# Kernel optimization log

Hardware: AMD Instinct MI355X
Metric: run time of the kernel (lower is better)

Reference implementation:

```python
import jax, jax.numpy as jnp
import numpy as np
import math

B, C, H, W = 4, 256, 64, 64
E = 96  # embed_dim
SOFTMAX_SCALE = 10.0
RESIDUAL_SCALE_INIT = 0.1


def conv1x1(w, x):
    # w: [out_c, in_c], x: [b, in_c, h, w] -> [b, out_c, h, w]
    return jnp.einsum('oc,bchw->bohw', w, x)


def setup_inputs() -> dict:
    key = jax.random.key(0)
    ks = jax.random.split(key, 12)
    s = 0.02
    return {
        'x': jax.random.normal(ks[0], (B, C, H, W), jnp.float32),
        'mask': jax.random.uniform(ks[1], (B, 1, H, W), jnp.float32),
        'ln_gamma': jnp.ones((C,), jnp.float32),
        'ln_beta': jnp.zeros((C,), jnp.float32),
        'wq': jax.random.normal(ks[2], (E, C), jnp.float32) * s,
        'wk': jax.random.normal(ks[3], (E, C), jnp.float32) * s,
        'wv': jax.random.normal(ks[4], (C, C), jnp.float32) * s,
        'w_out': jax.random.normal(ks[5], (C, C), jnp.float32) * s,
        'w_qm': jax.random.normal(ks[6], (E, 1), jnp.float32) * s,
        'wd1': jax.random.normal(ks[7], (C, 2 * C), jnp.float32) * s,
        'wd2': jax.random.normal(ks[8], (C, C), jnp.float32) * s,
        'wg': jax.random.normal(ks[9], (C, C + 1), jnp.float32) * s,
        'residual_scale': jnp.asarray(RESIDUAL_SCALE_INIT, jnp.float32),
    }


def reference(x, mask, ln_gamma, ln_beta, wq, wk, wv, w_out, w_qm, wd1, wd2, wg,
              residual_scale):
    b, c, h, w = x.shape
    n = h * w

    # ChannelLayerNorm: LayerNorm over channel dim
    mu = jnp.mean(x, axis=1, keepdims=True)
    var = jnp.mean((x - mu) ** 2, axis=1, keepdims=True)
    x_norm = (x - mu) / jnp.sqrt(var + 1e-5)
    x_norm = x_norm * ln_gamma[None, :, None, None] + ln_beta[None, :, None, None]

    # Q/K/V projections (1x1 convs), flatten to [b, n, d]
    q = conv1x1(wq, x_norm) + conv1x1(w_qm, mask)
    q = q.reshape(b, E, n).transpose(0, 2, 1)        # [b, n, E]
    k = conv1x1(wk, x_norm).reshape(b, E, n).transpose(0, 2, 1)  # [b, n, E]
    v = conv1x1(wv, x).reshape(b, c, n).transpose(0, 2, 1)       # [b, n, C]

    # cosine normalization (F.normalize with eps=1e-12)
    q = q / jnp.clip(jnp.linalg.norm(q, axis=-1, keepdims=True), 1e-12)
    k = k / jnp.clip(jnp.linalg.norm(k, axis=-1, keepdims=True), 1e-12)

    scale = SOFTMAX_SCALE / math.sqrt(E)
    attn = jnp.einsum('bqe,bke->bqk', q, k) * scale  # [b, n, n]

    # keys with mask >= 0.5 are invalid -> bias -10000
    invalid_keys = (mask.reshape(b, 1, n) >= 0.5)    # [b, 1, n]
    attn = jnp.where(invalid_keys, jnp.float32(-10000.0), attn)
    attn = jax.nn.softmax(attn, axis=-1)

    attended = jnp.einsum('bqk,bkc->bqc', attn, v)   # [b, n, C]
    attended = attended.transpose(0, 2, 1).reshape(b, c, h, w)
    attended = conv1x1(w_out, attended)

    # delta correction branch
    corr_in = jnp.concatenate([attended - x, x_norm * mask], axis=1)  # [b, 2C, h, w]
    hidden = jax.nn.gelu(conv1x1(wd1, corr_in), approximate=False)
    corrective = conv1x1(wd2, hidden)

    # MaskConditionedGate (assumed): sigmoid(1x1 conv over [corrective, mask])
    gate_in = jnp.concatenate([corrective, mask], axis=1)  # [b, C+1, h, w]
    gate = jax.nn.sigmoid(conv1x1(wg, gate_in)) * mask

    delta = jnp.tanh(residual_scale) * gate * corrective
    return x + delta
```

## Files before the change

kernel.cpp:

```cpp
#include <hip/hip_runtime.h>
#include <hip/hip_bf16.h>
#include <math.h>

#define BB 4
#define CC 256
#define NN 4096
#define EE 96
#define NTOT (BB*NN)

typedef __attribute__((ext_vector_type(8))) short bf16x8;
typedef __attribute__((ext_vector_type(4))) float f32x4;

__device__ __forceinline__ short f2bf(float x) {
    __hip_bfloat16 h = __float2bfloat16(x);
    return *reinterpret_cast<short*>(&h);
}
__device__ __forceinline__ float bf2f(short s) {
    unsigned int u = ((unsigned int)(unsigned short)s) << 16;
    float f;
    __builtin_memcpy(&f, &u, 4);
    return f;
}
__device__ __forceinline__ float gelu_exact(float v) {
    return 0.5f * v * (1.0f + erff(v * 0.70710678118654752f));
}
__device__ __forceinline__ void gld16(void* lds, const void* g) {
    __builtin_amdgcn_global_load_lds(
        (const __attribute__((address_space(1))) unsigned int*)g,
        (__attribute__((address_space(3))) unsigned int*)lds, 16, 0, 0);
}

#define OFF_WQ  0
#define OFF_WK  24576
#define OFF_WV  49152
#define OFF_WO  114688
#define OFF_WD1 180224
#define OFF_WD2 311296
#define OFF_WG  376832
#define OFF_WGL 442368
#define W16_TOTAL 442624

__global__ void wconv_kernel(const float* __restrict__ wq, const float* __restrict__ wk,
                             const float* __restrict__ wv, const float* __restrict__ wo,
                             const float* __restrict__ wd1, const float* __restrict__ wd2,
                             const float* __restrict__ wg, short* __restrict__ W16) {
    int i = blockIdx.x * 256 + threadIdx.x;
    if (i >= W16_TOTAL) return;
    float v;
    if      (i < OFF_WK)  v = wq[i];
    else if (i < OFF_WV)  v = wk[i - OFF_WK];
    else if (i < OFF_WO)  v = wv[i - OFF_WV];
    else if (i < OFF_WD1) v = wo[i - OFF_WO];
    else if (i < OFF_WD2) v = wd1[i - OFF_WD1];
    else if (i < OFF_WG)  v = wd2[i - OFF_WD2];
    else if (i < OFF_WGL) { int l = i - OFF_WG; v = wg[(l >> 8) * 257 + (l & 255)]; }
    else                  v = wg[(i - OFF_WGL) * 257 + 256];
    W16[i] = f2bf(v);
}

__global__ __launch_bounds__(256) void ln_kernel(
    const float* __restrict__ x, const float* __restrict__ gamma,
    const float* __restrict__ beta,
    short* __restrict__ Xt16, short* __restrict__ Xn16) {
    __shared__ float tile[256 * 33];
    __shared__ float psum[8][32], psq[8][32];
    __shared__ float mu_s[32], rs_s[32];
    __shared__ float gs[256], bs[256];
    const int b  = blockIdx.x >> 7;
    const int p0 = (blockIdx.x & 127) * 32;
    const int tid = threadIdx.x;
    const float* xb = x + (size_t)b * CC * NN;

    gs[tid] = gamma[tid];
    bs[tid] = beta[tid];
    #pragma unroll
    for (int i = 0; i < 8; ++i) {
        int idx = tid + i * 256;
        int c = idx >> 3, p4 = (idx & 7) * 4;
        float4 v = *(const float4*)&xb[(size_t)c * NN + p0 + p4];
        tile[c * 33 + p4]     = v.x;
        tile[c * 33 + p4 + 1] = v.y;
        tile[c * 33 + p4 + 2] = v.z;
        tile[c * 33 + p4 + 3] = v.w;
    }
    __syncthreads();
    {
        int col = tid & 31, part = tid >> 5;
        float s = 0.f, sq = 0.f;
        for (int r = part * 32; r < part * 32 + 32; ++r) {
            float v = tile[r * 33 + col];
            s += v; sq += v * v;
        }
        psum[part][col] = s; psq[part][col] = sq;
    }
    __syncthreads();
    if (tid < 32) {
        float S = 0.f, SQ = 0.f;
        #pragma unroll
        for (int j = 0; j < 8; ++j) { S += psum[j][tid]; SQ += psq[j][tid]; }
        float mu = S / 256.0f;
        float var = SQ / 256.0f - mu * mu;
        mu_s[tid] = mu;
        rs_s[tid] = rsqrtf(var + 1e-5f);
    }
    __syncthreads();
    size_t rowbase = ((size_t)b * NN + p0) * CC;
    #pragma unroll
    for (int i = 0; i < 4; ++i) {
        int idx = tid + i * 256;
        int p = idx >> 5, c8 = (idx & 31) * 8;
        float mu = mu_s[p], rcp = rs_s[p];
        bf16x8 xt, xn;
        #pragma unroll
        for (int j = 0; j < 8; ++j) {
            float v = tile[(c8 + j) * 33 + p];
            float n = (v - mu) * rcp * gs[c8 + j] + bs[c8 + j];
            xt[j] = f2bf(v); xn[j] = f2bf(n);
        }
        size_t o = rowbase + (size_t)p * CC + c8;
        *(bf16x8*)&Xt16[o] = xt;
        *(bf16x8*)&Xn16[o] = xn;
    }
}

__global__ __launch_bounds__(256) void qkproj_kernel(
    const short* __restrict__ Xn16, const short* __restrict__ W16,
    const float* __restrict__ mask, const float* __restrict__ w_qm,
    short* __restrict__ Q16, short* __restrict__ K16)
{
    const int tid = threadIdx.x;
    const int w = tid >> 6, lane = tid & 63, ln = lane & 15, quad = lane >> 4;
    const int m0 = blockIdx.x * 32 + (w & 1) * 16;
    const bool isQ = (w < 2);
    const int woff = isQ ? OFF_WQ : OFF_WK;

    f32x4 acc[6];
    #pragma unroll
    for (int i = 0; i < 6; ++i) acc[i] = (f32x4){0.f, 0.f, 0.f, 0.f};

    #pragma unroll
    for (int kt = 0; kt < 8; ++kt) {
        bf16x8 af = *(const bf16x8*)&Xn16[(size_t)(m0 + ln) * 256 + kt * 32 + quad * 8];
        #pragma unroll
        for (int nt = 0; nt < 6; ++nt) {
            bf16x8 bf = *(const bf16x8*)&W16[woff + (size_t)(nt * 16 + ln) * 256 + kt * 32 + quad * 8];
            acc[nt] = __builtin_amdgcn_mfma_f32_16x16x32_bf16(af, bf, acc[nt], 0, 0, 0);
        }
    }

    short* outp = isQ ? Q16 : K16;
    #pragma unroll
    for (int r = 0; r < 4; ++r) {
        int row = m0 + quad * 4 + r;
        float mrow = isQ ? mask[row] : 0.f;
        float vals[6];
        float ss = 0.f;
        #pragma unroll
        for (int nt = 0; nt < 6; ++nt) {
            float v = acc[nt][r];
            if (isQ) v += mrow * w_qm[nt * 16 + ln];
            vals[nt] = v;
            ss += v * v;
        }
        ss += __shfl_xor(ss, 1, 64); ss += __shfl_xor(ss, 2, 64);
        ss += __shfl_xor(ss, 4, 64); ss += __shfl_xor(ss, 8, 64);
        float sc = 1.0f / fmaxf(sqrtf(ss), 1e-12f);
        #pragma unroll
        for (int nt = 0; nt < 6; ++nt)
            outp[(size_t)row * EE + nt * 16 + ln] = f2bf(vals[nt] * sc);
    }
}

__global__ __launch_bounds__(256) void vproj_kernel(
    const short* __restrict__ Xt16, const short* __restrict__ W16,
    short* __restrict__ V16t)
{
    __shared__ short Vt[256 * 40];
    const int tid = threadIdx.x;
    const int w = tid >> 6, lane = tid & 63, ln = lane & 15, quad = lane >> 4;
    const int m0 = blockIdx.x * 32;
    const int wm = w >> 1, wn = w & 1;
    const int mrow = m0 + wm * 16;

    f32x4 acc[8];
    #pragma unroll
    for (int i = 0; i < 8; ++i) acc[i] = (f32x4){0.f, 0.f, 0.f, 0.f};

    #pragma unroll
    for (int kt = 0; kt < 8; ++kt) {
        bf16x8 af = *(const bf16x8*)&Xt16[(size_t)(mrow + ln) * 256 + kt * 32 + quad * 8];
        #pragma unroll
        for (int nt = 0; nt < 8; ++nt) {
            int col = wn * 128 + nt * 16 + ln;
            bf16x8 bf = *(const bf16x8*)&W16[OFF_WV + (size_t)col * 256 + kt * 32 + quad * 8];
            acc[nt] = __builtin_amdgcn_mfma_f32_16x16x32_bf16(af, bf, acc[nt], 0, 0, 0);
        }
    }
    #pragma unroll
    for (int nt = 0; nt < 8; ++nt) {
        int ch = wn * 128 + nt * 16 + ln;
        #pragma unroll
        for (int r = 0; r < 4; ++r)
            Vt[ch * 40 + wm * 16 + quad * 4 + r] = f2bf(acc[nt][r]);
    }
    __syncthreads();
    const int b = m0 >> 12, p0l = m0 & 4095;
    #pragma unroll
    for (int i = 0; i < 4; ++i) {
        int idx = tid + i * 256;
        int ch = idx >> 2, p8 = (idx & 3) * 8;
        *(bf16x8*)&V16t[((size_t)b * CC + ch) * NN + p0l + p8] =
            *(const bf16x8*)&Vt[ch * 40 + p8];
    }
}

__global__ __launch_bounds__(256, 3) void attn_kernel(
    const short* __restrict__ Q16, const short* __restrict__ K16,
    const short* __restrict__ V16t, const float* __restrict__ mask,
    short* __restrict__ Opart, float* __restrict__ Lpart)
{
    __shared__ short Ps[64 * 40];

    const int tid = threadIdx.x;
    const int w = tid >> 6, lane = tid & 63, ln = lane & 15, quad = lane >> 4;
    const int bidx = blockIdx.x;
    const int kg = bidx >> 8;
    const int qg = bidx & 255;
    const int b  = (qg & 7) >> 1;
    const int qt = ((qg >> 3) << 1) | (qg & 1);
    const int q0 = qt * 64;
    const size_t bN = (size_t)b * NN;
    const size_t bCC = (size_t)b * CC;
    const int kbase = kg * 1024;
    const float C1 = 1.02062072615966f;
    const int wbase = w * 64;

    bf16x8 qf[3];
    #pragma unroll
    for (int e = 0; e < 3; ++e)
        qf[e] = *(const bf16x8*)&Q16[(bN + q0 + w * 16 + ln) * EE + e * 32 + quad * 8];

    f32x4 acc[4][4];
    #pragma unroll
    for (int mt = 0; mt < 4; ++mt)
        #pragma unroll
        for (int nt = 0; nt < 4; ++nt) acc[mt][nt] = (f32x4){0.f, 0.f, 0.f, 0.f};
    float lsum[4] = {0.f, 0.f, 0.f, 0.f};

    for (int it = 0; it < 32; ++it) {
        const int k0 = kbase + it * 32;

        bf16x8 kf[6];
        #pragma unroll
        for (int e = 0; e < 3; ++e) {
            kf[2 * e]     = *(const bf16x8*)&K16[(bN + k0 + ln) * EE + e * 32 + quad * 8];
            kf[2 * e + 1] = *(const bf16x8*)&K16[(bN + k0 + 16 + ln) * EE + e * 32 + quad * 8];
        }
        bf16x8 vf[4];
        #pragma unroll
        for (int nt = 0; nt < 4; ++nt)
            vf[nt] = *(const bf16x8*)&V16t[(bCC + wbase + nt * 16 + ln) * NN + k0 + quad * 8];
        const float mk0 = mask[bN + k0 + ln];
        const float mk1 = mask[bN + k0 + 16 + ln];

        f32x4 s0 = (f32x4){0.f,0.f,0.f,0.f}, s1 = s0;
        __builtin_amdgcn_s_setprio(1);
        #pragma unroll
        for (int e = 0; e < 3; ++e) {
            s0 = __builtin_amdgcn_mfma_f32_16x16x32_bf16(qf[e], kf[2 * e],     s0, 0, 0, 0);
            s1 = __builtin_amdgcn_mfma_f32_16x16x32_bf16(qf[e], kf[2 * e + 1], s1, 0, 0, 0);
        }
        __builtin_amdgcn_s_setprio(0);
        const bool z0 = mk0 >= 0.5f;
        const bool z1 = mk1 >= 0.5f;
        #pragma unroll
        for (int r = 0; r < 4; ++r) {
            float p0 = z0 ? 0.f : __expf(fmaf(s0[r], C1, -C1));
            float p1 = z1 ? 0.f : __expf(fmaf(s1[r], C1, -C1));
            lsum[r] += p0 + p1;
            Ps[(w * 16 + quad * 4 + r) * 40 + ln]      = f2bf(p0);
            Ps[(w * 16 + quad * 4 + r) * 40 + 16 + ln] = f2bf(p1);
        }
        asm volatile("s_waitcnt lgkmcnt(0)" ::: "memory");
        __builtin_amdgcn_s_barrier();
        __builtin_amdgcn_sched_barrier(0);

        __builtin_amdgcn_s_setprio(1);
        #pragma unroll
        for (int mt = 0; mt < 4; ++mt) {
            bf16x8 pf = *(const bf16x8*)&Ps[(mt * 16 + ln) * 40 + quad * 8];
            #pragma unroll
            for (int nt = 0; nt < 4; ++nt)
                acc[mt][nt] = __builtin_amdgcn_mfma_f32_16x16x32_bf16(pf, vf[nt], acc[mt][nt], 0, 0, 0);
        }
        __builtin_amdgcn_s_setprio(0);
        asm volatile("s_waitcnt lgkmcnt(0)" ::: "memory");
        __builtin_amdgcn_s_barrier();
        __builtin_amdgcn_sched_barrier(0);
    }

    #pragma unroll
    for (int r = 0; r < 4; ++r) {
        float l = lsum[r];
        l += __shfl_xor(l, 1, 64); l += __shfl_xor(l, 2, 64);
        l += __shfl_xor(l, 4, 64); l += __shfl_xor(l, 8, 64);
        if (ln == 0)
            Lpart[(size_t)kg * NTOT + bN + q0 + w * 16 + quad * 4 + r] = l;
    }
    #pragma unroll
    for (int mt = 0; mt < 4; ++mt)
        #pragma unroll
        for (int nt = 0; nt < 4; ++nt)
            #pragma unroll
            for (int r = 0; r < 4; ++r)
                Opart[((size_t)kg * NTOT + bN + q0 + mt * 16 + quad * 4 + r) * 256
                      + wbase + nt * 16 + ln] = f2bf(acc[mt][nt][r]);
}

__global__ __launch_bounds__(256, 2) void epi_kernel(
    const short* __restrict__ Opart, const float* __restrict__ Lpart,
    const short* __restrict__ W16, const short* __restrict__ Xt16,
    const short* __restrict__ Xn16, const float* __restrict__ mask,
    const float* __restrict__ rs, const float* __restrict__ x,
    float* __restrict__ out)
{
    __shared__ char lds[54400];
    short* Olds  = (short*)lds;
    short* Hlds  = (short*)lds;
    short* Dlds  = (short*)(lds + 16896);
    short* Clds  = (short*)(lds + 16896);
    short* tileB = (short*)(lds + 33792);
    float* lsh   = (float*)(lds + 54272);

    const int tid = threadIdx.x;
    const int w = tid >> 6, lane = tid & 63, ln = lane & 15, quad = lane >> 4;
    const int wm = w >> 1, wn = w & 1;
    const int m0 = blockIdx.x * 32;
    const int b = m0 >> 12, p0l = m0 & 4095;

    if (tid < 32) {
        int g = m0 + tid;
        lsh[tid] = 1.0f / (Lpart[g] + Lpart[NTOT + g] + Lpart[2 * NTOT + g] + Lpart[3 * NTOT + g]);
    }
    __syncthreads();

    #pragma unroll
    for (int i = 0; i < 4; ++i) {
        int idx = tid + i * 256;
        int q = idx >> 5, ch8 = (idx & 31) * 8;
        size_t base = (size_t)(m0 + q) * 256 + ch8;
        bf16x8 a0 = *(const bf16x8*)&Opart[base];
        bf16x8 a1 = *(const bf16x8*)&Opart[(size_t)NTOT * 256 + base];
        bf16x8 a2 = *(const bf16x8*)&Opart[(size_t)2 * NTOT * 256 + base];
        bf16x8 a3 = *(const bf16x8*)&Opart[(size_t)3 * NTOT * 256 + base];
        float linv = lsh[q];
        bf16x8 o;
        #pragma unroll
        for (int e = 0; e < 8; ++e)
            o[e] = f2bf((bf2f(a0[e]) + bf2f(a1[e]) + bf2f(a2[e]) + bf2f(a3[e])) * linv);
        *(bf16x8*)&Olds[q * 264 + ch8] = o;
        bf16x8 xn = *(const bf16x8*)&Xn16[base];
        float mq = mask[m0 + q];
        bf16x8 xm;
        #pragma unroll
        for (int e = 0; e < 8; ++e) xm[e] = f2bf(bf2f(xn[e]) * mq);
        *(bf16x8*)&Dlds[q * 528 + 256 + ch8] = xm;
    }
    __syncthreads();

    {
        f32x4 acc[8];
        #pragma unroll
        for (int i = 0; i < 8; ++i) acc[i] = (f32x4){0.f, 0.f, 0.f, 0.f};
        #pragma unroll
        for (int kt = 0; kt < 8; ++kt) {
            bf16x8 af = *(const bf16x8*)&Olds[(wm * 16 + ln) * 264 + kt * 32 + quad * 8];
            #pragma unroll
            for (int nt = 0; nt < 8; ++nt) {
                int col = wn * 128 + nt * 16 + ln;
                bf16x8 bf = *(const bf16x8*)&W16[OFF_WO + (size_t)col * 256 + kt * 32 + quad * 8];
                acc[nt] = __builtin_amdgcn_mfma_f32_16x16x32_bf16(af, bf, acc[nt], 0, 0, 0);
            }
        }
        #pragma unroll
        for (int nt = 0; nt < 8; ++nt) {
            int col = wn * 128 + nt * 16 + ln;
            #pragma unroll
            for (int r = 0; r < 4; ++r) {
                int row = wm * 16 + quad * 4 + r;
                float v = acc[nt][r] - bf2f(Xt16[(size_t)(m0 + row) * 256 + col]);
                Dlds[row * 528 + col] = f2bf(v);
            }
        }
    }
    __syncthreads();

    {
        f32x4 acc[8];
        #pragma unroll
        for (int i = 0; i < 8; ++i) acc[i] = (f32x4){0.f, 0.f, 0.f, 0.f};
        #pragma unroll
        for (int kt = 0; kt < 16; ++kt) {
            bf16x8 af = *(const bf16x8*)&Dlds[(wm * 16 + ln) * 528 + kt * 32 + quad * 8];
            #pragma unroll
            for (int nt = 0; nt < 8; ++nt) {
                int col = wn * 128 + nt * 16 + ln;
                bf16x8 bf = *(const bf16x8*)&W16[OFF_WD1 + (size_t)col * 512 + kt * 32 + quad * 8];
                acc[nt] = __builtin_amdgcn_mfma_f32_16x16x32_bf16(af, bf, acc[nt], 0, 0, 0);
            }
        }
        __syncthreads();
        #pragma unroll
        for (int nt = 0; nt < 8; ++nt) {
            int col = wn * 128 + nt * 16 + ln;
            #pragma unroll
            for (int r = 0; r < 4; ++r) {
                int row = wm * 16 + quad * 4 + r;
                Hlds[row * 264 + col] = f2bf(gelu_exact(acc[nt][r]));
            }
        }
    }
    __syncthreads();

    {
        f32x4 acc[8];
        #pragma unroll
        for (int i = 0; i < 8; ++i) acc[i] = (f32x4){0.f, 0.f, 0.f, 0.f};
        #pragma unroll
        for (int kt = 0; kt < 8; ++kt) {
            bf16x8 af = *(const bf16x8*)&Hlds[(wm * 16 + ln) * 264 + kt * 32 + quad * 8];
            #pragma unroll
            for (int nt = 0; nt < 8; ++nt) {
                int col = wn * 128 + nt * 16 + ln;
                bf16x8 bf = *(const bf16x8*)&W16[OFF_WD2 + (size_t)col * 256 + kt * 32 + quad * 8];
                acc[nt] = __builtin_amdgcn_mfma_f32_16x16x32_bf16(af, bf, acc[nt], 0, 0, 0);
            }
        }
        __syncthreads();
        #pragma unroll
        for (int nt = 0; nt < 8; ++nt) {
            int col = wn * 128 + nt * 16 + ln;
            #pragma unroll
            for (int r = 0; r < 4; ++r) {
                int row = wm * 16 + quad * 4 + r;
                Clds[row * 264 + col] = f2bf(acc[nt][r]);
            }
        }
    }
    __syncthreads();

    {
        f32x4 acc[8];
        #pragma unroll
        for (int i = 0; i < 8; ++i) acc[i] = (f32x4){0.f, 0.f, 0.f, 0.f};
        #pragma unroll
        for (int kt = 0; kt < 8; ++kt) {
            bf16x8 af = *(const bf16x8*)&Clds[(wm * 16 + ln) * 264 + kt * 32 + quad * 8];
            #pragma unroll
            for (int nt = 0; nt < 8; ++nt) {
                int col = wn * 128 + nt * 16 + ln;
                bf16x8 bf = *(const bf16x8*)&W16[OFF_WG + (size_t)col * 256 + kt * 32 + quad * 8];
                acc[nt] = __builtin_amdgcn_mfma_f32_16x16x32_bf16(af, bf, acc[nt], 0, 0, 0);
            }
        }
        float trs = tanhf(rs[0]);
        #pragma unroll
        for (int nt = 0; nt < 8; ++nt) {
            int col = wn * 128 + nt * 16 + ln;
            float wgl = bf2f(W16[OFF_WGL + col]);
            #pragma unroll
            for (int r = 0; r < 4; ++r) {
                int row = wm * 16 + quad * 4 + r;
                float mrow = mask[m0 + row];
                float logit = acc[nt][r] + mrow * wgl;
                float gate = mrow / (1.0f + __expf(-logit));
                float corr = bf2f(Clds[row * 264 + col]);
                tileB[col * 40 + row] = f2bf(trs * gate * corr);
            }
        }
    }
    __syncthreads();

    #pragma unroll
    for (int i = 0; i < 4; ++i) {
        int idx = tid + i * 256;
        int ch = idx >> 2, p8 = (idx & 3) * 8;
        bf16x8 d = *(const bf16x8*)&tileB[ch * 40 + p8];
        size_t o = ((size_t)b * CC + ch) * NN + p0l + p8;
        float4 x0 = *(const float4*)&x[o];
        float4 x1 = *(const float4*)&x[o + 4];
        float4 o0, o1;
        o0.x = x0.x + bf2f(d[0]); o0.y = x0.y + bf2f(d[1]);
        o0.z = x0.z + bf2f(d[2]); o0.w = x0.w + bf2f(d[3]);
        o1.x = x1.x + bf2f(d[4]); o1.y = x1.y + bf2f(d[5]);
        o1.z = x1.z + bf2f(d[6]); o1.w = x1.w + bf2f(d[7]);
        *(float4*)&out[o] = o0;
        *(float4*)&out[o + 4] = o1;
    }
}

extern "C" void kernel_launch(void* const* d_in, const int* in_sizes, int n_in,
                              void* d_out, int out_size, void* d_ws, size_t ws_size,
                              hipStream_t stream) {
    const float* x     = (const float*)d_in[0];
    const float* mask  = (const float*)d_in[1];
    const float* gamma = (const float*)d_in[2];
    const float* beta  = (const float*)d_in[3];
    const float* wq    = (const float*)d_in[4];
    const float* wk    = (const float*)d_in[5];
    const float* wv    = (const float*)d_in[6];
    const float* w_out = (const float*)d_in[7];
    const float* w_qm  = (const float*)d_in[8];
    const float* wd1   = (const float*)d_in[9];
    const float* wd2   = (const float*)d_in[10];
    const float* wg    = (const float*)d_in[11];
    const float* rs    = (const float*)d_in[12];
    float* out = (float*)d_out;

    const size_t NC = (size_t)NTOT * CC;
    const size_t NE = (size_t)NTOT * EE;
    short* Xn16  = (short*)d_ws;
    short* Xt16  = Xn16 + NC;
    short* Q16   = Xt16 + NC;
    short* K16   = Q16 + NE;
    short* V16t  = K16 + NE;
    short* W16   = V16t + NC;
    short* Opart = W16 + W16_TOTAL;
    float* Lpart = (float*)(Opart + 4 * NC);

    wconv_kernel<<<(W16_TOTAL + 255) / 256, 256, 0, stream>>>(wq, wk, wv, w_out,
                                                              wd1, wd2, wg, W16);
    ln_kernel<<<512, 256, 0, stream>>>(x, gamma, beta, Xt16, Xn16);
    qkproj_kernel<<<512, 256, 0, stream>>>(Xn16, W16, mask, w_qm, Q16, K16);
    vproj_kernel<<<512, 256, 0, stream>>>(Xt16, W16, V16t);
    attn_kernel<<<1024, 256, 0, stream>>>(Q16, K16, V16t, mask, Opart, Lpart);
    epi_kernel<<<512, 256, 0, stream>>>(Opart, Lpart, W16, Xt16, Xn16, mask,
                                        rs, x, out);
}
```

Measured before the change: 331.6 us.

## Make attention waves independent with per-wave P tiles and register-prefetched K

The attention kernel now has each wave own 16 query rows across all 256 value channels, instead of sharing a 64-row P tile split by channel. Each wave keeps its own LDS slice for P, so both block-wide barriers per key step are gone. K and mask for the next step are software-prefetched into double-buffered registers through a 2x unrolled loop. The cost is that every wave loads all of V per step (4x more V traffic per block, relying on cache), plus more accumulator and V registers, and occupancy is lowered to 2 blocks per CU.

```diff
diff --git a/kernel.cpp b/kernel.cpp
--- a/kernel.cpp
+++ b/kernel.cpp
@@ -23,11 +23,6 @@
 }
 __device__ __forceinline__ float gelu_exact(float v) {
     return 0.5f * v * (1.0f + erff(v * 0.70710678118654752f));
-}
-__device__ __forceinline__ void gld16(void* lds, const void* g) {
-    __builtin_amdgcn_global_load_lds(
-        (const __attribute__((address_space(1))) unsigned int*)g,
-        (__attribute__((address_space(3))) unsigned int*)lds, 16, 0, 0);
 }
 
 #define OFF_WQ  0
@@ -214,12 +209,12 @@
     }
 }
 
-__global__ __launch_bounds__(256, 3) void attn_kernel(
+__global__ __launch_bounds__(256, 2) void attn_kernel(
     const short* __restrict__ Q16, const short* __restrict__ K16,
     const short* __restrict__ V16t, const float* __restrict__ mask,
     short* __restrict__ Opart, float* __restrict__ Lpart)
 {
-    __shared__ short Ps[64 * 40];
+    __shared__ short Ps[4 * 640];
 
     const int tid = threadIdx.x;
     const int w = tid >> 6, lane = tid & 63, ln = lane & 15, quad = lane >> 4;
@@ -233,44 +228,60 @@
     const size_t bCC = (size_t)b * CC;
     const int kbase = kg * 1024;
     const float C1 = 1.02062072615966f;
-    const int wbase = w * 64;
+    short* myPs = &Ps[w * 640];
 
     bf16x8 qf[3];
     #pragma unroll
     for (int e = 0; e < 3; ++e)
         qf[e] = *(const bf16x8*)&Q16[(bN + q0 + w * 16 + ln) * EE + e * 32 + quad * 8];
 
-    f32x4 acc[4][4];
-    #pragma unroll
-    for (int mt = 0; mt < 4; ++mt)
-        #pragma unroll
-        for (int nt = 0; nt < 4; ++nt) acc[mt][nt] = (f32x4){0.f, 0.f, 0.f, 0.f};
+    f32x4 acc[16];
+    #pragma unroll
+    for (int i = 0; i < 16; ++i) acc[i] = (f32x4){0.f, 0.f, 0.f, 0.f};
     float lsum[4] = {0.f, 0.f, 0.f, 0.f};
 
-    for (int it = 0; it < 32; ++it) {
+    bf16x8 kfA[6], kfB[6];
+    float mkA0, mkA1, mkB0, mkB1;
+    #pragma unroll
+    for (int e = 0; e < 3; ++e) {
+        kfA[2 * e]     = *(const bf16x8*)&K16[(bN + kbase + ln) * EE + e * 32 + quad * 8];
+        kfA[2 * e + 1] = *(const bf16x8*)&K16[(bN + kbase + 16 + ln) * EE + e * 32 + quad * 8];
+    }
+    mkA0 = mask[bN + kbase + ln];
+    mkA1 = mask[bN + kbase + 16 + ln];
+
+    auto iter = [&](int it, bf16x8* kfc, float mk0, float mk1,
+                    bf16x8* kfn, float& nmk0, float& nmk1) {
         const int k0 = kbase + it * 32;
 
-        bf16x8 kf[6];
-        #pragma unroll
-        for (int e = 0; e < 3; ++e) {
-            kf[2 * e]     = *(const bf16x8*)&K16[(bN + k0 + ln) * EE + e * 32 + quad * 8];
-            kf[2 * e + 1] = *(const bf16x8*)&K16[(bN + k0 + 16 + ln) * EE + e * 32 + quad * 8];
-        }
-        bf16x8 vf[4];
-        #pragma unroll
-        for (int nt = 0; nt < 4; ++nt)
-            vf[nt] = *(const bf16x8*)&V16t[(bCC + wbase + nt * 16 + ln) * NN + k0 + quad * 8];
-        const float mk0 = mask[bN + k0 + ln];
-        const float mk1 = mask[bN + k0 + 16 + ln];
+        bf16x8 vf0[8];
+        #pragma unroll
+        for (int nt = 0; nt < 8; ++nt)
+            vf0[nt] = *(const bf16x8*)&V16t[(bCC + nt * 16 + ln) * NN + k0 + quad * 8];
 
         f32x4 s0 = (f32x4){0.f,0.f,0.f,0.f}, s1 = s0;
         __builtin_amdgcn_s_setprio(1);
         #pragma unroll
         for (int e = 0; e < 3; ++e) {
-            s0 = __builtin_amdgcn_mfma_f32_16x16x32_bf16(qf[e], kf[2 * e],     s0, 0, 0, 0);
-            s1 = __builtin_amdgcn_mfma_f32_16x16x32_bf16(qf[e], kf[2 * e + 1], s1, 0, 0, 0);
+            s0 = __builtin_amdgcn_mfma_f32_16x16x32_bf16(qf[e], kfc[2 * e],     s0, 0, 0, 0);
+            s1 = __builtin_amdgcn_mfma_f32_16x16x32_bf16(qf[e], kfc[2 * e + 1], s1, 0, 0, 0);
         }
         __builtin_amdgcn_s_setprio(0);
+
+        bf16x8 vf1[8];
+        #pragma unroll
+        for (int nt = 0; nt < 8; ++nt)
+            vf1[nt] = *(const bf16x8*)&V16t[(bCC + (8 + nt) * 16 + ln) * NN + k0 + quad * 8];
+        const int itn = (it + 1 < 32) ? it + 1 : it;
+        const int k0n = kbase + itn * 32;
+        #pragma unroll
+        for (int e = 0; e < 3; ++e) {
+            kfn[2 * e]     = *(const bf16x8*)&K16[(bN + k0n + ln) * EE + e * 32 + quad * 8];
+            kfn[2 * e + 1] = *(const bf16x8*)&K16[(bN + k0n + 16 + ln) * EE + e * 32 + quad * 8];
+        }
+        nmk0 = mask[bN + k0n + ln];
+        nmk1 = mask[bN + k0n + 16 + ln];
+
         const bool z0 = mk0 >= 0.5f;
         const bool z1 = mk1 >= 0.5f;
         #pragma unroll
@@ -278,25 +289,25 @@
             float p0 = z0 ? 0.f : __expf(fmaf(s0[r], C1, -C1));
             float p1 = z1 ? 0.f : __expf(fmaf(s1[r], C1, -C1));
             lsum[r] += p0 + p1;
-            Ps[(w * 16 + quad * 4 + r) * 40 + ln]      = f2bf(p0);
-            Ps[(w * 16 + quad * 4 + r) * 40 + 16 + ln] = f2bf(p1);
-        }
-        asm volatile("s_waitcnt lgkmcnt(0)" ::: "memory");
-        __builtin_amdgcn_s_barrier();
-        __builtin_amdgcn_sched_barrier(0);
+            myPs[(quad * 4 + r) * 40 + ln]      = f2bf(p0);
+            myPs[(quad * 4 + r) * 40 + 16 + ln] = f2bf(p1);
+        }
+        bf16x8 pf = *(const bf16x8*)&myPs[ln * 40 + quad * 8];
 
         __builtin_amdgcn_s_setprio(1);
         #pragma unroll
-        for (int mt = 0; mt < 4; ++mt) {
-            bf16x8 pf = *(const bf16x8*)&Ps[(mt * 16 + ln) * 40 + quad * 8];
-            #pragma unroll
-            for (int nt = 0; nt < 4; ++nt)
-                acc[mt][nt] = __builtin_amdgcn_mfma_f32_16x16x32_bf16(pf, vf[nt], acc[mt][nt], 0, 0, 0);
-        }
+        for (int nt = 0; nt < 8; ++nt)
+            acc[nt] = __builtin_amdgcn_mfma_f32_16x16x32_bf16(pf, vf0[nt], acc[nt], 0, 0, 0);
+        #pragma unroll
+        for (int nt = 0; nt < 8; ++nt)
+            acc[8 + nt] = __builtin_amdgcn_mfma_f32_16x16x32_bf16(pf, vf1[nt], acc[8 + nt], 0, 0, 0);
         __builtin_amdgcn_s_setprio(0);
-        asm volatile("s_waitcnt lgkmcnt(0)" ::: "memory");
-        __builtin_amdgcn_s_barrier();
-        __builtin_amdgcn_sched_barrier(0);
+    };
+
+    #pragma unroll 1
+    for (int it2 = 0; it2 < 16; ++it2) {
+        iter(2 * it2,     kfA, mkA0, mkA1, kfB, mkB0, mkB1);
+        iter(2 * it2 + 1, kfB, mkB0, mkB1, kfA, mkA0, mkA1);
     }
 
     #pragma unroll
@@ -308,13 +319,11 @@
             Lpart[(size_t)kg * NTOT + bN + q0 + w * 16 + quad * 4 + r] = l;
     }
     #pragma unroll
-    for (int mt = 0; mt < 4; ++mt)
-        #pragma unroll
-        for (int nt = 0; nt < 4; ++nt)
-            #pragma unroll
-            for (int r = 0; r < 4; ++r)
-                Opart[((size_t)kg * NTOT + bN + q0 + mt * 16 + quad * 4 + r) * 256
-                      + wbase + nt * 16 + ln] = f2bf(acc[mt][nt][r]);
+    for (int nt = 0; nt < 16; ++nt)
+        #pragma unroll
+        for (int r = 0; r < 4; ++r)
+            Opart[((size_t)kg * NTOT + bN + q0 + w * 16 + quad * 4 + r) * 256
+                  + nt * 16 + ln] = f2bf(acc[nt][r]);
 }
 
 __global__ __launch_bounds__(256, 2) void epi_kernel(
```

New measurement: 490.3 us. 1.48x slower.
